# Performance work log

Measured on AMD Instinct MI355X. Metric: run time of the kernel, lower is better.

Reference implementation:

```python
import jax, jax.numpy as jnp
import numpy as np

NUM_CLASSES = 256
MARGIN = 0.3
EPS = 1e-12  # torch F.normalize eps


def setup_inputs() -> dict:
    key = jax.random.key(0)
    k1, k2 = jax.random.split(key)
    embeddings = jax.random.normal(k1, (65536, 512), dtype=jnp.float32)
    labels = jax.random.randint(k2, (65536,), 0, NUM_CLASSES)
    return {"embeddings": embeddings, "labels": labels}


def _l2_normalize(x):
    n = jnp.linalg.norm(x, axis=-1, keepdims=True)
    return x / jnp.maximum(n, EPS)


def reference(embeddings, labels):
    # emb_norm: (B, d)
    emb = _l2_normalize(embeddings)

    # Per-class segment mean -> centroids (C, d)
    counts = jax.ops.segment_sum(jnp.ones((emb.shape[0],), emb.dtype), labels,
                                 num_segments=NUM_CLASSES)          # (C,)
    sums = jax.ops.segment_sum(emb, labels, num_segments=NUM_CLASSES)  # (C, d)
    present = counts > 0                                              # (C,)
    cent = sums / jnp.maximum(counts, 1.0)[:, None]
    cent = _l2_normalize(cent)

    # Pairwise centroid euclidean distances (centroids are unit-norm).
    # Only used for argmin (no grad path), so stop_gradient for safety.
    cg = jax.lax.stop_gradient(cent)
    dist = jnp.sqrt(jnp.clip(2.0 - 2.0 * (cg @ cg.T), 0.0))           # (C, C)
    inf = jnp.asarray(jnp.inf, dist.dtype)
    dist = jnp.where(jnp.eye(NUM_CLASSES, dtype=bool), inf, dist)
    dist = jnp.where(present[None, :], dist, inf)  # empty classes can't be negatives
    nearest = jnp.argmin(dist, axis=1)                                # (C,)

    # Gather positive / nearest-negative centroid per sample
    pos_c = cent[labels]                 # (B, d)
    neg_c = cent[nearest[labels]]        # (B, d)
    d_pos = 1.0 - jnp.sum(emb * pos_c, axis=1)
    d_neg = 1.0 - jnp.sum(emb * neg_c, axis=1)
    terms = jax.nn.relu(d_pos - d_neg + MARGIN)                       # (B,)

    # Per-class mean of triplet terms, then mean over present classes
    loss_c = jax.ops.segment_sum(terms, labels, num_segments=NUM_CLASSES)
    loss_c = loss_c / jnp.maximum(counts, 1.0)
    n_present = jnp.maximum(jnp.sum(present.astype(emb.dtype)), 1.0)
    loss = jnp.sum(jnp.where(present, loss_c, 0.0)) / n_present
    return loss
```

## Files before the change

kernel.cpp:

```cpp
#include <hip/hip_runtime.h>
#include <math.h>

#define BROWS 65536
#define DIMS 512
#define NCLS 256
#define MARGIN 0.3f
#define EPSN 1e-12f
#define NSTRIP 64
#define SROWS 1024
#define LSPL 3
#define TSPL 8

__device__ __forceinline__ unsigned pk2(float lo, float hi) {
  unsigned a = __float_as_uint(lo), b = __float_as_uint(hi);
  a = (a + 0x7FFFu + ((a >> 16) & 1u)) >> 16;
  b = (b + 0x7FFFu + ((b >> 16) & 1u)) & 0xFFFF0000u;
  return a | b;
}
__device__ __forceinline__ float uplo(unsigned u) { return __uint_as_float(u << 16); }
__device__ __forceinline__ float uphi(unsigned u) { return __uint_as_float(u & 0xFFFF0000u); }

__global__ void __launch_bounds__(256) khist2(const int* __restrict__ labels,
                                              int* __restrict__ hist) {
  __shared__ int h[NCLS];
  int t = threadIdx.x, s = blockIdx.x;
  h[t] = 0;
  __syncthreads();
  int base = s * SROWS + t;
#pragma unroll
  for (int k = 0; k < SROWS / 256; ++k) atomicAdd(&h[labels[base + k * 256]], 1);
  __syncthreads();
  hist[s * NCLS + t] = h[t];
}

__global__ void __launch_bounds__(256) kscatter2(const int* __restrict__ labels,
                                                 const int* __restrict__ hist,
                                                 int* __restrict__ bases,
                                                 float* __restrict__ counts,
                                                 int* __restrict__ rowidx) {
  int t = threadIdx.x, s = blockIdx.x;
  int run = 0, myoff = 0;
  for (int s2 = 0; s2 < NSTRIP; ++s2) {
    int h = hist[s2 * NCLS + t];
    if (s2 < s) myoff += h;
    run += h;
  }
  __shared__ int sc[NCLS];
  sc[t] = run;
  __syncthreads();
  int v = sc[t];
  for (int off = 1; off < NCLS; off <<= 1) {
    int add = (t >= off) ? sc[t - off] : 0;
    __syncthreads();
    sc[t] = v = v + add;
    __syncthreads();
  }
  int excl = (t == 0) ? 0 : sc[t - 1];
  if (s == 0) {
    bases[t] = excl;
    counts[t] = (float)run;
  }
  __shared__ int loff[NCLS];
  __shared__ int cur[NCLS];
  loff[t] = excl + myoff;
  cur[t] = 0;
  __syncthreads();
  int rbase = s * SROWS + t;
#pragma unroll
  for (int k = 0; k < SROWS / 256; ++k) {
    int r = rbase + k * 256;
    int lab = labels[r];
    int lpos = atomicAdd(&cur[lab], 1);
    rowidx[loff[lab] + lpos] = r;
  }
}

__global__ void __launch_bounds__(256) ksumn(const float* __restrict__ emb,
                                             const int* __restrict__ rowidx,
                                             const int* __restrict__ bases,
                                             const float* __restrict__ counts,
                                             uint4* __restrict__ embn,
                                             float* __restrict__ partials) {
  int cls = blockIdx.x >> LSPL;
  int sp = blockIdx.x & ((1 << LSPL) - 1);
  int t = threadIdx.x, w = t >> 6, lane = t & 63;
  int base = bases[cls];
  int cnt = (int)counts[cls];
  int i0 = (cnt * sp) >> LSPL;
  int i1 = (cnt * (sp + 1)) >> LSPL;
  int n = i1 - i0;
  int j0 = i0 + ((n * w) >> 2);
  int j1 = i0 + ((n * (w + 1)) >> 2);
  const float4* ebase = reinterpret_cast<const float4*>(emb);
  int cq = lane * 2;
  float4 acc0 = make_float4(0.f, 0.f, 0.f, 0.f);
  float4 acc1 = make_float4(0.f, 0.f, 0.f, 0.f);
  int j = j0;
  for (; j + 4 <= j1; j += 4) {
    int r[4];
#pragma unroll
    for (int k = 0; k < 4; ++k) r[k] = rowidx[base + j + k];
    float4 a[4], b[4];
#pragma unroll
    for (int k = 0; k < 4; ++k) {
      const float4* p = ebase + (size_t)r[k] * (DIMS / 4) + cq;
      a[k] = p[0];
      b[k] = p[1];
    }
    float s[4];
#pragma unroll
    for (int k = 0; k < 4; ++k)
      s[k] = a[k].x*a[k].x + a[k].y*a[k].y + a[k].z*a[k].z + a[k].w*a[k].w
           + b[k].x*b[k].x + b[k].y*b[k].y + b[k].z*b[k].z + b[k].w*b[k].w;
#pragma unroll
    for (int off = 1; off < 64; off <<= 1) {
#pragma unroll
      for (int k = 0; k < 4; ++k) s[k] += __shfl_xor(s[k], off, 64);
    }
    float q[4];
#pragma unroll
    for (int k = 0; k < 4; ++k) q[k] = 1.0f / fmaxf(sqrtf(s[k]), EPSN);
#pragma unroll
    for (int k = 0; k < 4; ++k) {
      float nx0 = a[k].x * q[k], ny0 = a[k].y * q[k];
      float nz0 = a[k].z * q[k], nw0 = a[k].w * q[k];
      float nx1 = b[k].x * q[k], ny1 = b[k].y * q[k];
      float nz1 = b[k].z * q[k], nw1 = b[k].w * q[k];
      acc0.x += nx0; acc0.y += ny0; acc0.z += nz0; acc0.w += nw0;
      acc1.x += nx1; acc1.y += ny1; acc1.z += nz1; acc1.w += nw1;
      uint4 o;
      o.x = pk2(nx0, ny0); o.y = pk2(nz0, nw0);
      o.z = pk2(nx1, ny1); o.w = pk2(nz1, nw1);
      embn[(size_t)r[k] * (DIMS / 8) + lane] = o;
    }
  }
  for (; j < j1; ++j) {
    int r0 = rowidx[base + j];
    const float4* p = ebase + (size_t)r0 * (DIMS / 4) + cq;
    float4 a = p[0], b = p[1];
    float s = a.x*a.x + a.y*a.y + a.z*a.z + a.w*a.w
            + b.x*b.x + b.y*b.y + b.z*b.z + b.w*b.w;
#pragma unroll
    for (int off = 1; off < 64; off <<= 1) s += __shfl_xor(s, off, 64);
    float q0 = 1.0f / fmaxf(sqrtf(s), EPSN);
    float nx0 = a.x*q0, ny0 = a.y*q0, nz0 = a.z*q0, nw0 = a.w*q0;
    float nx1 = b.x*q0, ny1 = b.y*q0, nz1 = b.z*q0, nw1 = b.w*q0;
    acc0.x += nx0; acc0.y += ny0; acc0.z += nz0; acc0.w += nw0;
    acc1.x += nx1; acc1.y += ny1; acc1.z += nz1; acc1.w += nw1;
    uint4 o;
    o.x = pk2(nx0, ny0); o.y = pk2(nz0, nw0);
    o.z = pk2(nx1, ny1); o.w = pk2(nz1, nw1);
    embn[(size_t)r0 * (DIMS / 8) + lane] = o;
  }
  __shared__ float lds[4][DIMS];
  *reinterpret_cast<float4*>(&lds[w][lane * 8]) = acc0;
  *reinterpret_cast<float4*>(&lds[w][lane * 8 + 4]) = acc1;
  __syncthreads();
  float o0 = lds[0][t] + lds[1][t] + lds[2][t] + lds[3][t];
  float o1 = lds[0][t + 256] + lds[1][t + 256] + lds[2][t + 256] + lds[3][t + 256];
  float* outp = partials + ((size_t)sp * NCLS + cls) * DIMS;
  outp[t] = o0;
  outp[t + 256] = o1;
}

__global__ void __launch_bounds__(256) kcent(const float* __restrict__ partials,
                                             const float* __restrict__ counts,
                                             float* __restrict__ cent) {
  int cls = blockIdx.x, t = threadIdx.x;
  float s0 = 0.0f, s1 = 0.0f;
#pragma unroll
  for (int sp = 0; sp < (1 << LSPL); ++sp) {
    const float* p = partials + ((size_t)sp * NCLS + cls) * DIMS;
    s0 += p[t];
    s1 += p[t + 256];
  }
  float cm = fmaxf(counts[cls], 1.0f);
  float m0 = s0 / cm, m1 = s1 / cm;
  __shared__ float red[256];
  red[t] = m0 * m0 + m1 * m1;
  __syncthreads();
  for (int off = 128; off > 0; off >>= 1) {
    if (t < off) red[t] += red[t + off];
    __syncthreads();
  }
  float inv = 1.0f / fmaxf(sqrtf(red[0]), EPSN);
  cent[(size_t)cls * DIMS + t] = m0 * inv;
  cent[(size_t)cls * DIMS + t + 256] = m1 * inv;
}

__global__ void __launch_bounds__(256) knearest(const float* __restrict__ cent,
                                                const float* __restrict__ counts,
                                                int* __restrict__ nearest) {
  int i = blockIdx.x, j = threadIdx.x;
  __shared__ float ci[DIMS];
  ci[j] = cent[(size_t)i * DIMS + j];
  ci[j + 256] = cent[(size_t)i * DIMS + j + 256];
  __syncthreads();
  const float4* cj = reinterpret_cast<const float4*>(cent + (size_t)j * DIMS);
  float dot = 0.0f;
#pragma unroll 8
  for (int k = 0; k < DIMS / 4; ++k) {
    float4 v = cj[k];
    dot += v.x * ci[4*k] + v.y * ci[4*k+1] + v.z * ci[4*k+2] + v.w * ci[4*k+3];
  }
  float dist = sqrtf(fmaxf(2.0f - 2.0f * dot, 0.0f));
  bool valid = (j != i) && (counts[j] > 0.0f);
  float dv = valid ? dist : INFINITY;
  __shared__ float sd[256];
  __shared__ int si[256];
  sd[j] = dv; si[j] = j;
  __syncthreads();
  for (int off = 128; off > 0; off >>= 1) {
    if (j < off) {
      float o = sd[j + off]; int oi = si[j + off];
      if (o < sd[j] || (o == sd[j] && oi < si[j])) { sd[j] = o; si[j] = oi; }
    }
    __syncthreads();
  }
  if (j == 0) nearest[i] = si[0];
}

__global__ void __launch_bounds__(256) kterm2(const uint4* __restrict__ embn,
                                              const int* __restrict__ rowidx,
                                              const int* __restrict__ bases,
                                              const float* __restrict__ counts,
                                              const float* __restrict__ cent,
                                              const int* __restrict__ nearest,
                                              float* __restrict__ tsums) {
  int cls = blockIdx.x >> 3;
  int sp = blockIdx.x & (TSPL - 1);
  int t = threadIdx.x, w = t >> 6, lane = t & 63;
  int base = bases[cls];
  int cnt = (int)counts[cls];
  int ng = nearest[cls];
  int cq = lane * 2;
  const float4* pp = reinterpret_cast<const float4*>(cent + (size_t)cls * DIMS) + cq;
  const float4* pn = reinterpret_cast<const float4*>(cent + (size_t)ng * DIMS) + cq;
  float4 P0 = pp[0], P1 = pp[1], N0 = pn[0], N1 = pn[1];
  float4 d0 = make_float4(N0.x - P0.x, N0.y - P0.y, N0.z - P0.z, N0.w - P0.w);
  float4 d1 = make_float4(N1.x - P1.x, N1.y - P1.y, N1.z - P1.z, N1.w - P1.w);
  int i0 = (cnt * sp) / TSPL;
  int i1 = (cnt * (sp + 1)) / TSPL;
  int n = i1 - i0;
  int j0 = i0 + ((n * w) >> 2);
  int j1 = i0 + ((n * (w + 1)) >> 2);
  float tsum = 0.0f;
  int j = j0;
  for (; j + 8 <= j1; j += 8) {
    int r[8];
#pragma unroll
    for (int k = 0; k < 8; ++k) r[k] = rowidx[base + j + k];
    uint4 v[8];
#pragma unroll
    for (int k = 0; k < 8; ++k) v[k] = embn[(size_t)r[k] * (DIMS / 8) + lane];
    float s[8];
#pragma unroll
    for (int k = 0; k < 8; ++k)
      s[k] = uplo(v[k].x)*d0.x + uphi(v[k].x)*d0.y + uplo(v[k].y)*d0.z + uphi(v[k].y)*d0.w
           + uplo(v[k].z)*d1.x + uphi(v[k].z)*d1.y + uplo(v[k].w)*d1.z + uphi(v[k].w)*d1.w;
#pragma unroll
    for (int off = 1; off < 64; off <<= 1) {
#pragma unroll
      for (int k = 0; k < 8; ++k) s[k] += __shfl_xor(s[k], off, 64);
    }
#pragma unroll
    for (int k = 0; k < 8; ++k) tsum += fmaxf(s[k] + MARGIN, 0.0f);
  }
  for (; j < j1; ++j) {
    int r0 = rowidx[base + j];
    uint4 v = embn[(size_t)r0 * (DIMS / 8) + lane];
    float s = uplo(v.x)*d0.x + uphi(v.x)*d0.y + uplo(v.y)*d0.z + uphi(v.y)*d0.w
            + uplo(v.z)*d1.x + uphi(v.z)*d1.y + uplo(v.w)*d1.z + uphi(v.w)*d1.w;
#pragma unroll
    for (int off = 1; off < 64; off <<= 1) s += __shfl_xor(s, off, 64);
    tsum += fmaxf(s + MARGIN, 0.0f);
  }
  __shared__ float sred[4];
  if (lane == 0) sred[w] = tsum;
  __syncthreads();
  if (t == 0) tsums[blockIdx.x] = sred[0] + sred[1] + sred[2] + sred[3];
}

__global__ void __launch_bounds__(256) kfinal(const float* __restrict__ counts,
                                              const float* __restrict__ tsums,
                                              float* __restrict__ out) {
  int t = threadIdx.x;
  float cnt = counts[t];
  bool present = cnt > 0.0f;
  float ls = 0.0f;
#pragma unroll
  for (int k = 0; k < TSPL; ++k) ls += tsums[t * TSPL + k];
  float v = present ? ls / fmaxf(cnt, 1.0f) : 0.0f;
  float np = present ? 1.0f : 0.0f;
  __shared__ float sv[256], sp[256];
  sv[t] = v; sp[t] = np;
  __syncthreads();
  for (int off = 128; off > 0; off >>= 1) {
    if (t < off) { sv[t] += sv[t + off]; sp[t] += sp[t + off]; }
    __syncthreads();
  }
  if (t == 0) out[0] = sv[0] / fmaxf(sp[0], 1.0f);
}

extern "C" void kernel_launch(void* const* d_in, const int* in_sizes, int n_in,
                              void* d_out, int out_size, void* d_ws, size_t ws_size,
                              hipStream_t stream) {
  const float* emb = (const float*)d_in[0];
  const int* labels = (const int*)d_in[1];
  float* out = (float*)d_out;

  char* ws = (char*)d_ws;
  size_t off = 0;
  auto alloc = [&](size_t bytes) {
    char* p = ws + off;
    off += (bytes + 255) & ~(size_t)255;
    return p;
  };
  int*   hist    = (int*)alloc((size_t)NSTRIP * NCLS * 4);
  int*   bases   = (int*)alloc((size_t)NCLS * 4);
  float* counts  = (float*)alloc((size_t)NCLS * 4);
  float* cent    = (float*)alloc((size_t)NCLS * DIMS * 4);
  int*   nearest = (int*)alloc((size_t)NCLS * 4);
  int*   rowidx  = (int*)alloc((size_t)BROWS * 4);
  float* tsums   = (float*)alloc((size_t)NCLS * TSPL * 4);
  float* partials= (float*)alloc(((size_t)NCLS * DIMS * 4) << LSPL);
  uint4* embn    = (uint4*)alloc((size_t)BROWS * DIMS * 2);

  khist2<<<NSTRIP, 256, 0, stream>>>(labels, hist);
  kscatter2<<<NSTRIP, 256, 0, stream>>>(labels, hist, bases, counts, rowidx);
  ksumn<<<NCLS << LSPL, 256, 0, stream>>>(emb, rowidx, bases, counts, embn, partials);
  kcent<<<NCLS, 256, 0, stream>>>(partials, counts, cent);
  knearest<<<NCLS, 256, 0, stream>>>(cent, counts, nearest);
  kterm2<<<NCLS * TSPL, 256, 0, stream>>>(embn, rowidx, bases, counts, cent, nearest, tsums);
  kfinal<<<1, 256, 0, stream>>>(counts, tsums, out);
}
```

Baseline: 253.0 us.

## Store per-row inverse norms instead of bf16 normalized copy; reread fp32 embeddings

Instead of writing a bf16 copy of the normalized embeddings in the centroid-sum kernel, only the per-row inverse norm is stored. The triplet-term kernel re-reads the original fp32 rows and scales the reduced dot product by the inverse norm. This removes a large intermediate write and the bf16 pack/unpack work. In exchange, the second pass reads twice as many bytes per row and relies on cache reuse of the original input.

```diff
diff --git a/kernel.cpp b/kernel.cpp
--- a/kernel.cpp
+++ b/kernel.cpp
@@ -10,15 +10,6 @@
 #define SROWS 1024
 #define LSPL 3
 #define TSPL 8
-
-__device__ __forceinline__ unsigned pk2(float lo, float hi) {
-  unsigned a = __float_as_uint(lo), b = __float_as_uint(hi);
-  a = (a + 0x7FFFu + ((a >> 16) & 1u)) >> 16;
-  b = (b + 0x7FFFu + ((b >> 16) & 1u)) & 0xFFFF0000u;
-  return a | b;
-}
-__device__ __forceinline__ float uplo(unsigned u) { return __uint_as_float(u << 16); }
-__device__ __forceinline__ float uphi(unsigned u) { return __uint_as_float(u & 0xFFFF0000u); }
 
 __global__ void __launch_bounds__(256) khist2(const int* __restrict__ labels,
                                               int* __restrict__ hist) {
@@ -79,7 +70,7 @@
                                              const int* __restrict__ rowidx,
                                              const int* __restrict__ bases,
                                              const float* __restrict__ counts,
-                                             uint4* __restrict__ embn,
+                                             float* __restrict__ invnorm,
                                              float* __restrict__ partials) {
   int cls = blockIdx.x >> LSPL;
   int sp = blockIdx.x & ((1 << LSPL) - 1);
@@ -120,18 +111,16 @@
     float q[4];
 #pragma unroll
     for (int k = 0; k < 4; ++k) q[k] = 1.0f / fmaxf(sqrtf(s[k]), EPSN);
+    if (lane == 0) {
+      invnorm[r[0]] = q[0]; invnorm[r[1]] = q[1];
+      invnorm[r[2]] = q[2]; invnorm[r[3]] = q[3];
+    }
 #pragma unroll
     for (int k = 0; k < 4; ++k) {
-      float nx0 = a[k].x * q[k], ny0 = a[k].y * q[k];
-      float nz0 = a[k].z * q[k], nw0 = a[k].w * q[k];
-      float nx1 = b[k].x * q[k], ny1 = b[k].y * q[k];
-      float nz1 = b[k].z * q[k], nw1 = b[k].w * q[k];
-      acc0.x += nx0; acc0.y += ny0; acc0.z += nz0; acc0.w += nw0;
-      acc1.x += nx1; acc1.y += ny1; acc1.z += nz1; acc1.w += nw1;
-      uint4 o;
-      o.x = pk2(nx0, ny0); o.y = pk2(nz0, nw0);
-      o.z = pk2(nx1, ny1); o.w = pk2(nz1, nw1);
-      embn[(size_t)r[k] * (DIMS / 8) + lane] = o;
+      acc0.x += a[k].x * q[k]; acc0.y += a[k].y * q[k];
+      acc0.z += a[k].z * q[k]; acc0.w += a[k].w * q[k];
+      acc1.x += b[k].x * q[k]; acc1.y += b[k].y * q[k];
+      acc1.z += b[k].z * q[k]; acc1.w += b[k].w * q[k];
     }
   }
   for (; j < j1; ++j) {
@@ -143,14 +132,9 @@
 #pragma unroll
     for (int off = 1; off < 64; off <<= 1) s += __shfl_xor(s, off, 64);
     float q0 = 1.0f / fmaxf(sqrtf(s), EPSN);
-    float nx0 = a.x*q0, ny0 = a.y*q0, nz0 = a.z*q0, nw0 = a.w*q0;
-    float nx1 = b.x*q0, ny1 = b.y*q0, nz1 = b.z*q0, nw1 = b.w*q0;
-    acc0.x += nx0; acc0.y += ny0; acc0.z += nz0; acc0.w += nw0;
-    acc1.x += nx1; acc1.y += ny1; acc1.z += nz1; acc1.w += nw1;
-    uint4 o;
-    o.x = pk2(nx0, ny0); o.y = pk2(nz0, nw0);
-    o.z = pk2(nx1, ny1); o.w = pk2(nz1, nw1);
-    embn[(size_t)r0 * (DIMS / 8) + lane] = o;
+    if (lane == 0) invnorm[r0] = q0;
+    acc0.x += a.x * q0; acc0.y += a.y * q0; acc0.z += a.z * q0; acc0.w += a.w * q0;
+    acc1.x += b.x * q0; acc1.y += b.y * q0; acc1.z += b.z * q0; acc1.w += b.w * q0;
   }
   __shared__ float lds[4][DIMS];
   *reinterpret_cast<float4*>(&lds[w][lane * 8]) = acc0;
@@ -220,7 +204,8 @@
   if (j == 0) nearest[i] = si[0];
 }
 
-__global__ void __launch_bounds__(256) kterm2(const uint4* __restrict__ embn,
+__global__ void __launch_bounds__(256) kterm2(const float* __restrict__ emb,
+                                              const float* __restrict__ invnorm,
                                               const int* __restrict__ rowidx,
                                               const int* __restrict__ bases,
                                               const float* __restrict__ counts,
@@ -244,36 +229,46 @@
   int n = i1 - i0;
   int j0 = i0 + ((n * w) >> 2);
   int j1 = i0 + ((n * (w + 1)) >> 2);
+  const float4* ebase = reinterpret_cast<const float4*>(emb);
   float tsum = 0.0f;
   int j = j0;
-  for (; j + 8 <= j1; j += 8) {
-    int r[8];
-#pragma unroll
-    for (int k = 0; k < 8; ++k) r[k] = rowidx[base + j + k];
-    uint4 v[8];
-#pragma unroll
-    for (int k = 0; k < 8; ++k) v[k] = embn[(size_t)r[k] * (DIMS / 8) + lane];
-    float s[8];
-#pragma unroll
-    for (int k = 0; k < 8; ++k)
-      s[k] = uplo(v[k].x)*d0.x + uphi(v[k].x)*d0.y + uplo(v[k].y)*d0.z + uphi(v[k].y)*d0.w
-           + uplo(v[k].z)*d1.x + uphi(v[k].z)*d1.y + uplo(v[k].w)*d1.z + uphi(v[k].w)*d1.w;
+  for (; j + 4 <= j1; j += 4) {
+    int r[4];
+#pragma unroll
+    for (int k = 0; k < 4; ++k) r[k] = rowidx[base + j + k];
+    float inv[4];
+#pragma unroll
+    for (int k = 0; k < 4; ++k) inv[k] = invnorm[r[k]];
+    float4 a[4], b[4];
+#pragma unroll
+    for (int k = 0; k < 4; ++k) {
+      const float4* p = ebase + (size_t)r[k] * (DIMS / 4) + cq;
+      a[k] = p[0];
+      b[k] = p[1];
+    }
+    float s[4];
+#pragma unroll
+    for (int k = 0; k < 4; ++k)
+      s[k] = a[k].x*d0.x + a[k].y*d0.y + a[k].z*d0.z + a[k].w*d0.w
+           + b[k].x*d1.x + b[k].y*d1.y + b[k].z*d1.z + b[k].w*d1.w;
 #pragma unroll
     for (int off = 1; off < 64; off <<= 1) {
 #pragma unroll
-      for (int k = 0; k < 8; ++k) s[k] += __shfl_xor(s[k], off, 64);
-    }
-#pragma unroll
-    for (int k = 0; k < 8; ++k) tsum += fmaxf(s[k] + MARGIN, 0.0f);
+      for (int k = 0; k < 4; ++k) s[k] += __shfl_xor(s[k], off, 64);
+    }
+#pragma unroll
+    for (int k = 0; k < 4; ++k) tsum += fmaxf(s[k] * inv[k] + MARGIN, 0.0f);
   }
   for (; j < j1; ++j) {
     int r0 = rowidx[base + j];
-    uint4 v = embn[(size_t)r0 * (DIMS / 8) + lane];
-    float s = uplo(v.x)*d0.x + uphi(v.x)*d0.y + uplo(v.y)*d0.z + uphi(v.y)*d0.w
-            + uplo(v.z)*d1.x + uphi(v.z)*d1.y + uplo(v.w)*d1.z + uphi(v.w)*d1.w;
+    float inv0 = invnorm[r0];
+    const float4* p = ebase + (size_t)r0 * (DIMS / 4) + cq;
+    float4 a = p[0], b = p[1];
+    float s = a.x*d0.x + a.y*d0.y + a.z*d0.z + a.w*d0.w
+            + b.x*d1.x + b.y*d1.y + b.z*d1.z + b.w*d1.w;
 #pragma unroll
     for (int off = 1; off < 64; off <<= 1) s += __shfl_xor(s, off, 64);
-    tsum += fmaxf(s + MARGIN, 0.0f);
+    tsum += fmaxf(s * inv0 + MARGIN, 0.0f);
   }
   __shared__ float sred[4];
   if (lane == 0) sred[w] = tsum;
@@ -322,15 +317,16 @@
   float* cent    = (float*)alloc((size_t)NCLS * DIMS * 4);
   int*   nearest = (int*)alloc((size_t)NCLS * 4);
   int*   rowidx  = (int*)alloc((size_t)BROWS * 4);
+  float* invnorm = (float*)alloc((size_t)BROWS * 4);
   float* tsums   = (float*)alloc((size_t)NCLS * TSPL * 4);
   float* partials= (float*)alloc(((size_t)NCLS * DIMS * 4) << LSPL);
-  uint4* embn    = (uint4*)alloc((size_t)BROWS * DIMS * 2);
 
   khist2<<<NSTRIP, 256, 0, stream>>>(labels, hist);
   kscatter2<<<NSTRIP, 256, 0, stream>>>(labels, hist, bases, counts, rowidx);
-  ksumn<<<NCLS << LSPL, 256, 0, stream>>>(emb, rowidx, bases, counts, embn, partials);
+  ksumn<<<NCLS << LSPL, 256, 0, stream>>>(emb, rowidx, bases, counts, invnorm, partials);
   kcent<<<NCLS, 256, 0, stream>>>(partials, counts, cent);
   knearest<<<NCLS, 256, 0, stream>>>(cent, counts, nearest);
-  kterm2<<<NCLS * TSPL, 256, 0, stream>>>(embn, rowidx, bases, counts, cent, nearest, tsums);
+  kterm2<<<NCLS * TSPL, 256, 0, stream>>>(emb, invnorm, rowidx, bases, counts,
+                                          cent, nearest, tsums);
   kfinal<<<1, 256, 0, stream>>>(counts, tsums, out);
 }
```

Result: no change. 248.3 us, median of 2 (-1.9%).
